# Kernel optimization log

Hardware: AMD Instinct MI355X
Metric: run time of the kernel (lower is better)

Reference implementation:

```python
import jax, jax.numpy as jnp
import numpy as np

N = 100000   # nodes
E = 1600000  # edges (before self loops)
IN, HID, OUT = 128, 128, 64


def setup_inputs() -> dict:
    key = jax.random.key(0)
    ks = jax.random.split(key, 5)
    x = jax.random.normal(ks[0], (N, IN), dtype=jnp.float32)
    edge_index = jax.random.randint(ks[1], (2, E), 0, N, dtype=jnp.int32)
    W1 = jax.random.normal(ks[2], (IN, HID), dtype=jnp.float32) * (1.0 / np.sqrt(IN))
    b1 = jnp.zeros((HID,), dtype=jnp.float32)
    W2 = jax.random.normal(ks[3], (HID, OUT), dtype=jnp.float32) * (1.0 / np.sqrt(HID))
    b2 = jnp.zeros((OUT,), dtype=jnp.float32)
    return {"x": x, "edge_index": edge_index, "W1": W1, "b1": b1, "W2": W2, "b2": b2}


def _gcn_conv(x, W, b, src, dst, norm):
    # linear transform first (small GEMM), then normalized scatter-add aggregation
    h = x @ W                                   # [N, d_out]
    msg = h[src] * norm[:, None]                # [E+N, d_out] gathered messages
    agg = jax.ops.segment_sum(msg, dst, num_segments=N)
    return agg + b


def reference(x, edge_index, W1, b1, W2, b2):
    loops = jnp.arange(N, dtype=edge_index.dtype)
    src = jnp.concatenate([edge_index[0], loops])   # add self loops (PyG GCNConv default)
    dst = jnp.concatenate([edge_index[1], loops])
    # symmetric normalization D^{-1/2} (A+I) D^{-1/2}
    deg = jax.ops.segment_sum(jnp.ones_like(dst, dtype=x.dtype), dst, num_segments=N)
    dinv = jnp.where(deg > 0, jax.lax.rsqrt(deg), 0.0)
    norm = dinv[src] * dinv[dst]                # [E+N]

    h = _gcn_conv(x, W1, b1, src, dst, norm)
    h = jax.nn.relu(h)
    out = _gcn_conv(h, W2, b2, src, dst, norm)
    return out
```

## Files before the change

kernel.cpp:

```cpp
#include <hip/hip_runtime.h>
#include <hip/hip_bf16.h>

#define IN_DIM  128
#define HID_DIM 128
#define OUT_DIM 64

typedef unsigned short ushort_t;
struct ushort4_t { ushort_t x, y, z, w; };
typedef __attribute__((ext_vector_type(8))) short bf16x8;
typedef __attribute__((ext_vector_type(4))) float f32x4;

__device__ __forceinline__ float bf2f(ushort_t u) {
    return __uint_as_float(((unsigned int)u) << 16);
}
__device__ __forceinline__ short f2bf_s(float v) {
    __hip_bfloat16 t = __float2bfloat16(v);
    return *(short*)&t;
}
__device__ __forceinline__ unsigned int pack2(float a, float b) {
    return ((unsigned int)(ushort_t)f2bf_s(b) << 16) | (ushort_t)f2bf_s(a);
}

__global__ __launch_bounds__(256, 2) void fused_gemm1_count(
        const float* __restrict__ x, const float* __restrict__ W,
        unsigned int* __restrict__ h,
        const int* __restrict__ dst, int* __restrict__ cnt, int* __restrict__ rank,
        int N, int E, int NT) {
    const int bid = blockIdx.x;
    const int tid = threadIdx.x;

    if (bid & 1) {
        const int lane = tid & 63;
        const int m    = lane & 15;
        const int quad = lane >> 4;
        const int gw   = (bid >> 1) * 4 + (tid >> 6);
        const int NW   = 1024;

        bf16x8 a[8][4];
        #pragma unroll
        for (int ct = 0; ct < 8; ++ct)
            #pragma unroll
            for (int kc = 0; kc < 4; ++kc)
                #pragma unroll
                for (int j = 0; j < 8; ++j)
                    a[ct][kc][j] = f2bf_s(W[(size_t)(kc * 32 + quad * 8 + j) * HID_DIM + ct * 16 + m]);

        for (int t = gw; t < NT; t += NW) {
            const int n0 = t * 16;
            int node = n0 + m; if (node >= N) node = N - 1;
            const float* xr = x + (size_t)node * IN_DIM + quad * 8;
            f32x4 acc[8];
            #pragma unroll
            for (int ct = 0; ct < 8; ++ct) acc[ct] = (f32x4){0.f, 0.f, 0.f, 0.f};
            #pragma unroll
            for (int kc = 0; kc < 4; ++kc) {
                const float4 v0 = *(const float4*)(xr + kc * 32);
                const float4 v1 = *(const float4*)(xr + kc * 32 + 4);
                bf16x8 b;
                b[0] = f2bf_s(v0.x); b[1] = f2bf_s(v0.y); b[2] = f2bf_s(v0.z); b[3] = f2bf_s(v0.w);
                b[4] = f2bf_s(v1.x); b[5] = f2bf_s(v1.y); b[6] = f2bf_s(v1.z); b[7] = f2bf_s(v1.w);
                #pragma unroll
                for (int ct = 0; ct < 8; ++ct)
                    acc[ct] = __builtin_amdgcn_mfma_f32_16x16x32_bf16(a[ct][kc], b, acc[ct], 0, 0, 0);
            }
            if (n0 + m < N) {
                unsigned int* o = h + (size_t)(n0 + m) * (HID_DIM / 2) + quad * 2;
                #pragma unroll
                for (int ct = 0; ct < 8; ++ct) {
                    uint2 pv;
                    pv.x = pack2(acc[ct][0], acc[ct][1]);
                    pv.y = pack2(acc[ct][2], acc[ct][3]);
                    *(uint2*)(o + ct * 8) = pv;
                }
            }
        }
    } else {
        const int ct = (bid >> 1) * 256 + tid;
        const int CT = 256 * 256;
        const int nq = E >> 2;
        const int4* d4 = (const int4*)dst;
        for (int q = ct; q < nq; q += CT) {
            const int4 d = d4[q];
            int4 r;
            r.x = atomicAdd(&cnt[d.x], 1);
            r.y = atomicAdd(&cnt[d.y], 1);
            r.z = atomicAdd(&cnt[d.z], 1);
            r.w = atomicAdd(&cnt[d.w], 1);
            ((int4*)rank)[q] = r;
        }
        for (int e = (nq << 2) + ct; e < E; e += CT)
            rank[e] = atomicAdd(&cnt[dst[e]], 1);
    }
}

__global__ void scan_partial(const int* __restrict__ cnt, int* __restrict__ bsum,
                             float* __restrict__ dinv, int N) {
    __shared__ int wsum[4];
    const int t = threadIdx.x;
    const int base = blockIdx.x * 2048 + t * 8;
    int s = 0;
    #pragma unroll
    for (int i = 0; i < 8; ++i) {
        if (base + i < N) {
            const int c = cnt[base + i];
            dinv[base + i] = rsqrtf((float)(c + 1));
            s += (c + 3) & ~3;
        }
    }
    #pragma unroll
    for (int off = 32; off > 0; off >>= 1) s += __shfl_down(s, off);
    const int lane = t & 63, w = t >> 6;
    if (lane == 0) wsum[w] = s;
    __syncthreads();
    if (t == 0) bsum[blockIdx.x] = wsum[0] + wsum[1] + wsum[2] + wsum[3];
}

__global__ void scan_write(const int* __restrict__ cnt, const int* __restrict__ bsum,
                           int* __restrict__ row_start, int2* __restrict__ pack, int N) {
    __shared__ int wsum[4];
    __shared__ int blockoff;
    const int t = threadIdx.x;
    if (t < 64) {
        int a = 0;
        for (int idx = t; idx < blockIdx.x; idx += 64) a += bsum[idx];
        #pragma unroll
        for (int off = 32; off > 0; off >>= 1) a += __shfl_down(a, off);
        if (t == 0) blockoff = a;
    }
    const int base = blockIdx.x * 2048 + t * 8;
    int c[8], v[8];
    #pragma unroll
    for (int i = 0; i < 8; ++i) {
        c[i] = (base + i < N) ? cnt[base + i] : 0;
        v[i] = (c[i] + 3) & ~3;
    }
    int s = v[0] + v[1] + v[2] + v[3] + v[4] + v[5] + v[6] + v[7];
    const int lane = t & 63, w = t >> 6;
    int incl = s;
    #pragma unroll
    for (int off = 1; off < 64; off <<= 1) {
        int u = __shfl_up(incl, off);
        if (lane >= off) incl += u;
    }
    if (lane == 63) wsum[w] = incl;
    __syncthreads();
    int woff = 0;
    for (int i = 0; i < w; ++i) woff += wsum[i];
    int run = blockoff + woff + (incl - s);
    const int2 zr = {0, 0};
    #pragma unroll
    for (int i = 0; i < 8; ++i) {
        if (base + i < N) {
            row_start[base + i] = run;
            for (int p = c[i]; p < v[i]; ++p) pack[run + p] = zr;
            run += v[i];
        }
    }
}

__global__ void fill_pack4(const int* __restrict__ src, const int* __restrict__ dst,
                           const int* __restrict__ rank, const int* __restrict__ row_start,
                           const float* __restrict__ dinv, int E, int2* __restrict__ pack) {
    const int q = blockIdx.x * blockDim.x + threadIdx.x;
    const int nq = E >> 2;
    if (q < nq) {
        const int4 s = ((const int4*)src)[q];
        const int4 d = ((const int4*)dst)[q];
        const int4 r = ((const int4*)rank)[q];
        int2 p;
        p.x = s.x; p.y = __float_as_int(dinv[s.x] * dinv[d.x]);
        pack[row_start[d.x] + r.x] = p;
        p.x = s.y; p.y = __float_as_int(dinv[s.y] * dinv[d.y]);
        pack[row_start[d.y] + r.y] = p;
        p.x = s.z; p.y = __float_as_int(dinv[s.z] * dinv[d.z]);
        pack[row_start[d.z] + r.z] = p;
        p.x = s.w; p.y = __float_as_int(dinv[s.w] * dinv[d.w]);
        pack[row_start[d.w] + r.w] = p;
    }
    if (q == 0) {
        for (int e = nq << 2; e < E; ++e) {
            int2 p;
            p.x = src[e]; p.y = __float_as_int(dinv[src[e]] * dinv[dst[e]]);
            pack[row_start[dst[e]] + rank[e]] = p;
        }
    }
}

__global__ __launch_bounds__(256) void gemm2_mfma(
        const ushort_t* __restrict__ agg,
        const float* __restrict__ W2, unsigned int* __restrict__ h2,
        int N, int NT, int NW) {
    const int tid  = threadIdx.x;
    const int lane = tid & 63;
    const int m    = lane & 15;
    const int quad = lane >> 4;
    const int gw   = blockIdx.x * 4 + (tid >> 6);

    bf16x8 a[4][4];
    #pragma unroll
    for (int ct = 0; ct < 4; ++ct)
        #pragma unroll
        for (int kc = 0; kc < 4; ++kc)
            #pragma unroll
            for (int j = 0; j < 8; ++j)
                a[ct][kc][j] = f2bf_s(W2[(size_t)(kc * 32 + quad * 8 + j) * OUT_DIM + ct * 16 + m]);

    for (int t = gw; t < NT; t += NW) {
        const int n0 = t * 16;
        int node = n0 + m; if (node >= N) node = N - 1;
        const ushort_t* ar = agg + (size_t)node * HID_DIM + quad * 8;
        f32x4 acc[4];
        #pragma unroll
        for (int ct = 0; ct < 4; ++ct) acc[ct] = (f32x4){0.f, 0.f, 0.f, 0.f};
        #pragma unroll
        for (int kc = 0; kc < 4; ++kc) {
            const bf16x8 b = *(const bf16x8*)(ar + kc * 32);
            #pragma unroll
            for (int ct = 0; ct < 4; ++ct)
                acc[ct] = __builtin_amdgcn_mfma_f32_16x16x32_bf16(a[ct][kc], b, acc[ct], 0, 0, 0);
        }
        if (n0 + m < N) {
            unsigned int* o = h2 + (size_t)(n0 + m) * (OUT_DIM / 2) + quad * 2;
            #pragma unroll
            for (int ct = 0; ct < 4; ++ct) {
                uint2 pv;
                pv.x = pack2(acc[ct][0], acc[ct][1]);
                pv.y = pack2(acc[ct][2], acc[ct][3]);
                *(uint2*)(o + ct * 8) = pv;
            }
        }
    }
}

template<int D, bool BF16_OUT, bool RELU>
__global__ void gather_bf16(const ushort_t* __restrict__ h, const int2* __restrict__ pack,
                            const int* __restrict__ row_start, const int* __restrict__ cnt,
                            const float* __restrict__ dinv, const float* __restrict__ bias,
                            int N, void* __restrict__ outv) {
    const int TPN = D / 4;
    const int NPB = 256 / TPN;
    const int t = threadIdx.x;
    const int node = blockIdx.x * NPB + t / TPN;
    if (node >= N) return;
    const int f = (t & (TPN - 1)) * 4;
    const float dd = dinv[node];

    const ushort4_t self = *(const ushort4_t*)(h + (size_t)node * D + f);
    const float sn = dd * dd;
    float4 acc;
    acc.x = bf2f(self.x) * sn; acc.y = bf2f(self.y) * sn;
    acc.z = bf2f(self.z) * sn; acc.w = bf2f(self.w) * sn;
    const float4 bv = *(const float4*)(bias + f);
    acc.x += bv.x; acc.y += bv.y; acc.z += bv.z; acc.w += bv.w;

    const int2* pk = pack + row_start[node];
    const int cpad = (cnt[node] + 3) & ~3;
    for (int e = 0; e < cpad; e += 4) {
        const int4 a = *(const int4*)(pk + e);
        const int4 b = *(const int4*)(pk + e + 2);
        {
            const ushort4_t v = *(const ushort4_t*)(h + (size_t)a.x * D + f);
            const float n = __int_as_float(a.y);
            acc.x += bf2f(v.x) * n; acc.y += bf2f(v.y) * n;
            acc.z += bf2f(v.z) * n; acc.w += bf2f(v.w) * n;
        }
        {
            const ushort4_t v = *(const ushort4_t*)(h + (size_t)a.z * D + f);
            const float n = __int_as_float(a.w);
            acc.x += bf2f(v.x) * n; acc.y += bf2f(v.y) * n;
            acc.z += bf2f(v.z) * n; acc.w += bf2f(v.w) * n;
        }
        {
            const ushort4_t v = *(const ushort4_t*)(h + (size_t)b.x * D + f);
            const float n = __int_as_float(b.y);
            acc.x += bf2f(v.x) * n; acc.y += bf2f(v.y) * n;
            acc.z += bf2f(v.z) * n; acc.w += bf2f(v.w) * n;
        }
        {
            const ushort4_t v = *(const ushort4_t*)(h + (size_t)b.z * D + f);
            const float n = __int_as_float(b.w);
            acc.x += bf2f(v.x) * n; acc.y += bf2f(v.y) * n;
            acc.z += bf2f(v.z) * n; acc.w += bf2f(v.w) * n;
        }
    }
    if (RELU) {
        acc.x = fmaxf(acc.x, 0.f); acc.y = fmaxf(acc.y, 0.f);
        acc.z = fmaxf(acc.z, 0.f); acc.w = fmaxf(acc.w, 0.f);
    }
    if (BF16_OUT) {
        unsigned int* out = (unsigned int*)outv;
        uint2 pv;
        pv.x = pack2(acc.x, acc.y);
        pv.y = pack2(acc.z, acc.w);
        *(uint2*)(out + ((size_t)node * D + f) / 2) = pv;
    } else {
        float* out = (float*)outv;
        *(float4*)(out + (size_t)node * D + f) = acc;
    }
}

extern "C" void kernel_launch(void* const* d_in, const int* in_sizes, int n_in,
                              void* d_out, int out_size, void* d_ws, size_t ws_size,
                              hipStream_t stream) {
    const float* x   = (const float*)d_in[0];
    const int*   ei  = (const int*)  d_in[1];
    const float* W1  = (const float*)d_in[2];
    const float* b1  = (const float*)d_in[3];
    const float* W2  = (const float*)d_in[4];
    const float* b2  = (const float*)d_in[5];
    float* out = (float*)d_out;

    const int N = in_sizes[0] / IN_DIM;
    const int E = in_sizes[1] / 2;
    const int* src = ei;
    const int* dst = ei + E;

    const int PACK_CAP = E + 4 * N;
    float* dinv      = (float*)d_ws;
    int*   cnt       = (int*)(dinv + N);
    int*   row_start = cnt + N;
    int*   bsum      = row_start + N;
    size_t off       = (size_t)(3 * N + 1024);
    off = (off + 3) & ~(size_t)3;
    int2*  pack      = (int2*)((int*)d_ws + off);
    unsigned int* h1 = (unsigned int*)(pack + PACK_CAP);
    unsigned int* agg1 = h1 + (size_t)N * (HID_DIM / 2);
    int*   rank      = (int*)agg1;
    unsigned int* h2 = h1;

    const int B = 256;
    const int S = (N + 2047) / 2048;
    const int NT = (N + 15) / 16;

    hipMemsetAsync(cnt, 0, (size_t)N * sizeof(int), stream);
    fused_gemm1_count<<<512, 256, 0, stream>>>(x, W1, h1, dst, cnt, rank, N, E, NT);

    scan_partial<<<S, 256, 0, stream>>>(cnt, bsum, dinv, N);
    scan_write<<<S, 256, 0, stream>>>(cnt, bsum, row_start, pack, N);

    fill_pack4<<<((E >> 2) + B - 1) / B, B, 0, stream>>>(src, dst, rank, row_start, dinv, E, pack);

    gather_bf16<HID_DIM, true, true><<<(N + 7) / 8, 256, 0, stream>>>(
        (const ushort_t*)h1, pack, row_start, cnt, dinv, b1, N, (void*)agg1);

    gemm2_mfma<<<768, 256, 0, stream>>>(
        (const ushort_t*)agg1, W2, h2, N, NT, 768 * 4);

    gather_bf16<OUT_DIM, false, false><<<(N + 15) / 16, 256, 0, stream>>>(
        (const ushort_t*)h2, pack, row_start, cnt, dinv, b2, N, (void*)out);
}
```

Before: 312.2 us.

## Fuse GEMM1, degree count, scan and CSR fill into one persistent kernel

Merges the fused GEMM1/count kernel, both scan kernels and the pack-fill kernel into a single persistent 512-block kernel, separated by atomic-counter grid barriers. This removes three kernel launches and the gaps between them. The barrier counter shares the cnt memset. It relies on all 512 blocks being co-resident, or it will deadlock. The gather loop is also unrolled to process eight edges per iteration for more memory-level parallelism.

```diff
diff --git a/kernel.cpp b/kernel.cpp
--- a/kernel.cpp
+++ b/kernel.cpp
@@ -21,13 +21,30 @@
     return ((unsigned int)(ushort_t)f2bf_s(b) << 16) | (ushort_t)f2bf_s(a);
 }
 
-__global__ __launch_bounds__(256, 2) void fused_gemm1_count(
+__device__ __forceinline__ void grid_barrier(int* bar, int epoch, int nb) {
+    __syncthreads();
+    if (threadIdx.x == 0) {
+        __threadfence();
+        __hip_atomic_fetch_add(bar, 1, __ATOMIC_RELEASE, __HIP_MEMORY_SCOPE_AGENT);
+        while (__hip_atomic_load(bar, __ATOMIC_ACQUIRE, __HIP_MEMORY_SCOPE_AGENT) < epoch * nb)
+            __builtin_amdgcn_s_sleep(100);
+        __threadfence();
+    }
+    __syncthreads();
+}
+
+__global__ __launch_bounds__(256, 2) void megakernel(
         const float* __restrict__ x, const float* __restrict__ W,
         unsigned int* __restrict__ h,
-        const int* __restrict__ dst, int* __restrict__ cnt, int* __restrict__ rank,
-        int N, int E, int NT) {
+        const int* __restrict__ src, const int* __restrict__ dst,
+        int* __restrict__ cnt, int* __restrict__ rank,
+        float* __restrict__ dinv, int* __restrict__ bsum,
+        int* __restrict__ row_start, int2* __restrict__ pack,
+        int* __restrict__ bar,
+        int N, int E, int NT, int S) {
     const int bid = blockIdx.x;
     const int tid = threadIdx.x;
+    const int NB  = 512;
 
     if (bid & 1) {
         const int lane = tid & 63;
@@ -91,97 +108,98 @@
         for (int e = (nq << 2) + ct; e < E; e += CT)
             rank[e] = atomicAdd(&cnt[dst[e]], 1);
     }
-}
-
-__global__ void scan_partial(const int* __restrict__ cnt, int* __restrict__ bsum,
-                             float* __restrict__ dinv, int N) {
-    __shared__ int wsum[4];
-    const int t = threadIdx.x;
-    const int base = blockIdx.x * 2048 + t * 8;
-    int s = 0;
-    #pragma unroll
-    for (int i = 0; i < 8; ++i) {
-        if (base + i < N) {
-            const int c = cnt[base + i];
-            dinv[base + i] = rsqrtf((float)(c + 1));
-            s += (c + 3) & ~3;
-        }
-    }
-    #pragma unroll
-    for (int off = 32; off > 0; off >>= 1) s += __shfl_down(s, off);
-    const int lane = t & 63, w = t >> 6;
-    if (lane == 0) wsum[w] = s;
-    __syncthreads();
-    if (t == 0) bsum[blockIdx.x] = wsum[0] + wsum[1] + wsum[2] + wsum[3];
-}
-
-__global__ void scan_write(const int* __restrict__ cnt, const int* __restrict__ bsum,
-                           int* __restrict__ row_start, int2* __restrict__ pack, int N) {
-    __shared__ int wsum[4];
-    __shared__ int blockoff;
-    const int t = threadIdx.x;
-    if (t < 64) {
-        int a = 0;
-        for (int idx = t; idx < blockIdx.x; idx += 64) a += bsum[idx];
-        #pragma unroll
-        for (int off = 32; off > 0; off >>= 1) a += __shfl_down(a, off);
-        if (t == 0) blockoff = a;
-    }
-    const int base = blockIdx.x * 2048 + t * 8;
-    int c[8], v[8];
-    #pragma unroll
-    for (int i = 0; i < 8; ++i) {
-        c[i] = (base + i < N) ? cnt[base + i] : 0;
-        v[i] = (c[i] + 3) & ~3;
-    }
-    int s = v[0] + v[1] + v[2] + v[3] + v[4] + v[5] + v[6] + v[7];
-    const int lane = t & 63, w = t >> 6;
-    int incl = s;
-    #pragma unroll
-    for (int off = 1; off < 64; off <<= 1) {
-        int u = __shfl_up(incl, off);
-        if (lane >= off) incl += u;
-    }
-    if (lane == 63) wsum[w] = incl;
-    __syncthreads();
-    int woff = 0;
-    for (int i = 0; i < w; ++i) woff += wsum[i];
-    int run = blockoff + woff + (incl - s);
-    const int2 zr = {0, 0};
-    #pragma unroll
-    for (int i = 0; i < 8; ++i) {
-        if (base + i < N) {
-            row_start[base + i] = run;
-            for (int p = c[i]; p < v[i]; ++p) pack[run + p] = zr;
-            run += v[i];
-        }
-    }
-}
-
-__global__ void fill_pack4(const int* __restrict__ src, const int* __restrict__ dst,
-                           const int* __restrict__ rank, const int* __restrict__ row_start,
-                           const float* __restrict__ dinv, int E, int2* __restrict__ pack) {
-    const int q = blockIdx.x * blockDim.x + threadIdx.x;
-    const int nq = E >> 2;
-    if (q < nq) {
-        const int4 s = ((const int4*)src)[q];
-        const int4 d = ((const int4*)dst)[q];
-        const int4 r = ((const int4*)rank)[q];
-        int2 p;
-        p.x = s.x; p.y = __float_as_int(dinv[s.x] * dinv[d.x]);
-        pack[row_start[d.x] + r.x] = p;
-        p.x = s.y; p.y = __float_as_int(dinv[s.y] * dinv[d.y]);
-        pack[row_start[d.y] + r.y] = p;
-        p.x = s.z; p.y = __float_as_int(dinv[s.z] * dinv[d.z]);
-        pack[row_start[d.z] + r.z] = p;
-        p.x = s.w; p.y = __float_as_int(dinv[s.w] * dinv[d.w]);
-        pack[row_start[d.w] + r.w] = p;
-    }
-    if (q == 0) {
-        for (int e = nq << 2; e < E; ++e) {
+
+    grid_barrier(bar, 1, NB);
+
+    if (bid < S) {
+        __shared__ int wsum2[4];
+        const int base = bid * 2048 + tid * 8;
+        int s = 0;
+        #pragma unroll
+        for (int i = 0; i < 8; ++i) {
+            if (base + i < N) {
+                const int c = cnt[base + i];
+                dinv[base + i] = rsqrtf((float)(c + 1));
+                s += (c + 3) & ~3;
+            }
+        }
+        #pragma unroll
+        for (int off = 32; off > 0; off >>= 1) s += __shfl_down(s, off);
+        const int lane = tid & 63, w = tid >> 6;
+        if (lane == 0) wsum2[w] = s;
+        __syncthreads();
+        if (tid == 0) bsum[bid] = wsum2[0] + wsum2[1] + wsum2[2] + wsum2[3];
+    }
+
+    grid_barrier(bar, 2, NB);
+
+    if (bid < S) {
+        __shared__ int wsum3[4];
+        __shared__ int blockoff;
+        if (tid < 64) {
+            int a = 0;
+            for (int idx = tid; idx < bid; idx += 64) a += bsum[idx];
+            #pragma unroll
+            for (int off = 32; off > 0; off >>= 1) a += __shfl_down(a, off);
+            if (tid == 0) blockoff = a;
+        }
+        const int base = bid * 2048 + tid * 8;
+        int c[8], v[8];
+        #pragma unroll
+        for (int i = 0; i < 8; ++i) {
+            c[i] = (base + i < N) ? cnt[base + i] : 0;
+            v[i] = (c[i] + 3) & ~3;
+        }
+        int s = v[0] + v[1] + v[2] + v[3] + v[4] + v[5] + v[6] + v[7];
+        const int lane = tid & 63, w = tid >> 6;
+        int incl = s;
+        #pragma unroll
+        for (int off = 1; off < 64; off <<= 1) {
+            int u = __shfl_up(incl, off);
+            if (lane >= off) incl += u;
+        }
+        if (lane == 63) wsum3[w] = incl;
+        __syncthreads();
+        int woff = 0;
+        for (int i = 0; i < w; ++i) woff += wsum3[i];
+        int run = blockoff + woff + (incl - s);
+        const int2 zr = {0, 0};
+        #pragma unroll
+        for (int i = 0; i < 8; ++i) {
+            if (base + i < N) {
+                row_start[base + i] = run;
+                for (int p = c[i]; p < v[i]; ++p) pack[run + p] = zr;
+                run += v[i];
+            }
+        }
+    }
+
+    grid_barrier(bar, 3, NB);
+
+    {
+        const int gtid = bid * 256 + tid;
+        const int GT = NB * 256;
+        const int nq = E >> 2;
+        for (int q = gtid; q < nq; q += GT) {
+            const int4 s = ((const int4*)src)[q];
+            const int4 d = ((const int4*)dst)[q];
+            const int4 r = ((const int4*)rank)[q];
             int2 p;
-            p.x = src[e]; p.y = __float_as_int(dinv[src[e]] * dinv[dst[e]]);
-            pack[row_start[dst[e]] + rank[e]] = p;
+            p.x = s.x; p.y = __float_as_int(dinv[s.x] * dinv[d.x]);
+            pack[row_start[d.x] + r.x] = p;
+            p.x = s.y; p.y = __float_as_int(dinv[s.y] * dinv[d.y]);
+            pack[row_start[d.y] + r.y] = p;
+            p.x = s.z; p.y = __float_as_int(dinv[s.z] * dinv[d.z]);
+            pack[row_start[d.z] + r.z] = p;
+            p.x = s.w; p.y = __float_as_int(dinv[s.w] * dinv[d.w]);
+            pack[row_start[d.w] + r.w] = p;
+        }
+        if (gtid == 0) {
+            for (int e = nq << 2; e < E; ++e) {
+                int2 p;
+                p.x = src[e]; p.y = __float_as_int(dinv[src[e]] * dinv[dst[e]]);
+                pack[row_start[dst[e]] + rank[e]] = p;
+            }
         }
     }
 }
@@ -231,6 +249,13 @@
         }
     }
 }
+
+#define GREC(P, HI) do { \
+        const ushort4_t v = *(const ushort4_t*)(h + (size_t)(HI ? (P).z : (P).x) * D + f); \
+        const float n = __int_as_float(HI ? (P).w : (P).y); \
+        acc.x += bf2f(v.x) * n; acc.y += bf2f(v.y) * n; \
+        acc.z += bf2f(v.z) * n; acc.w += bf2f(v.w) * n; \
+    } while (0)
 
 template<int D, bool BF16_OUT, bool RELU>
 __global__ void gather_bf16(const ushort_t* __restrict__ h, const int2* __restrict__ pack,
@@ -255,33 +280,22 @@
 
     const int2* pk = pack + row_start[node];
     const int cpad = (cnt[node] + 3) & ~3;
-    for (int e = 0; e < cpad; e += 4) {
-        const int4 a = *(const int4*)(pk + e);
-        const int4 b = *(const int4*)(pk + e + 2);
-        {
-            const ushort4_t v = *(const ushort4_t*)(h + (size_t)a.x * D + f);
-            const float n = __int_as_float(a.y);
-            acc.x += bf2f(v.x) * n; acc.y += bf2f(v.y) * n;
-            acc.z += bf2f(v.z) * n; acc.w += bf2f(v.w) * n;
-        }
-        {
-            const ushort4_t v = *(const ushort4_t*)(h + (size_t)a.z * D + f);
-            const float n = __int_as_float(a.w);
-            acc.x += bf2f(v.x) * n; acc.y += bf2f(v.y) * n;
-            acc.z += bf2f(v.z) * n; acc.w += bf2f(v.w) * n;
-        }
-        {
-            const ushort4_t v = *(const ushort4_t*)(h + (size_t)b.x * D + f);
-            const float n = __int_as_float(b.y);
-            acc.x += bf2f(v.x) * n; acc.y += bf2f(v.y) * n;
-            acc.z += bf2f(v.z) * n; acc.w += bf2f(v.w) * n;
-        }
-        {
-            const ushort4_t v = *(const ushort4_t*)(h + (size_t)b.z * D + f);
-            const float n = __int_as_float(b.w);
-            acc.x += bf2f(v.x) * n; acc.y += bf2f(v.y) * n;
-            acc.z += bf2f(v.z) * n; acc.w += bf2f(v.w) * n;
-        }
+    int e = 0;
+    for (; e + 8 <= cpad; e += 8) {
+        const int4 p0 = *(const int4*)(pk + e);
+        const int4 p1 = *(const int4*)(pk + e + 2);
+        const int4 p2 = *(const int4*)(pk + e + 4);
+        const int4 p3 = *(const int4*)(pk + e + 6);
+        GREC(p0, 0); GREC(p0, 1);
+        GREC(p1, 0); GREC(p1, 1);
+        GREC(p2, 0); GREC(p2, 1);
+        GREC(p3, 0); GREC(p3, 1);
+    }
+    if (e < cpad) {
+        const int4 p0 = *(const int4*)(pk + e);
+        const int4 p1 = *(const int4*)(pk + e + 2);
+        GREC(p0, 0); GREC(p0, 1);
+        GREC(p1, 0); GREC(p1, 1);
     }
     if (RELU) {
         acc.x = fmaxf(acc.x, 0.f); acc.y = fmaxf(acc.y, 0.f);
@@ -318,9 +332,10 @@
     const int PACK_CAP = E + 4 * N;
     float* dinv      = (float*)d_ws;
     int*   cnt       = (int*)(dinv + N);
-    int*   row_start = cnt + N;
+    int*   bar       = cnt + N;
+    int*   row_start = bar + 16;
     int*   bsum      = row_start + N;
-    size_t off       = (size_t)(3 * N + 1024);
+    size_t off       = (size_t)(3 * N + 16 + 1024);
     off = (off + 3) & ~(size_t)3;
     int2*  pack      = (int2*)((int*)d_ws + off);
     unsigned int* h1 = (unsigned int*)(pack + PACK_CAP);
@@ -328,17 +343,12 @@
     int*   rank      = (int*)agg1;
     unsigned int* h2 = h1;
 
-    const int B = 256;
     const int S = (N + 2047) / 2048;
     const int NT = (N + 15) / 16;
 
-    hipMemsetAsync(cnt, 0, (size_t)N * sizeof(int), stream);
-    fused_gemm1_count<<<512, 256, 0, stream>>>(x, W1, h1, dst, cnt, rank, N, E, NT);
-
-    scan_partial<<<S, 256, 0, stream>>>(cnt, bsum, dinv, N);
-    scan_write<<<S, 256, 0, stream>>>(cnt, bsum, row_start, pack, N);
-
-    fill_pack4<<<((E >> 2) + B - 1) / B, B, 0, stream>>>(src, dst, rank, row_start, dinv, E, pack);
+    hipMemsetAsync(cnt, 0, ((size_t)N + 16) * sizeof(int), stream);
+    megakernel<<<512, 256, 0, stream>>>(x, W1, h1, src, dst, cnt, rank,
+                                        dinv, bsum, row_start, pack, bar, N, E, NT, S);
 
     gather_bf16<HID_DIM, true, true><<<(N + 7) / 8, 256, 0, stream>>>(
         (const ushort_t*)h1, pack, row_start, cnt, dinv, b1, N, (void*)agg1);
```

Result: slower. 581.8 us (+86.3%).

## Shard degree-count atomics across shadow counter arrays and unroll gather loop

Applied to the files above, without the earlier changes.

Splits the per-destination degree counters into 8 shadow copies chosen by thread block, so atomic increments contend less. The scan then sums the shadows and writes a per-shadow base offset, which fill_pack4 uses to place each edge in the CSR. The gather loop is also unrolled to handle 8 edges per iteration. The cost is a larger memset and extra reads and writes of 8N-sized arrays in the scan kernels.

```diff
diff --git a/kernel.cpp b/kernel.cpp
--- a/kernel.cpp
+++ b/kernel.cpp
@@ -4,6 +4,7 @@
 #define IN_DIM  128
 #define HID_DIM 128
 #define OUT_DIM 64
+#define NSHADOW 8
 
 typedef unsigned short ushort_t;
 struct ushort4_t { ushort_t x, y, z, w; };
@@ -24,7 +25,7 @@
 __global__ __launch_bounds__(256, 2) void fused_gemm1_count(
         const float* __restrict__ x, const float* __restrict__ W,
         unsigned int* __restrict__ h,
-        const int* __restrict__ dst, int* __restrict__ cnt, int* __restrict__ rank,
+        const int* __restrict__ dst, int* __restrict__ scnt, int* __restrict__ rank,
         int N, int E, int NT) {
     const int bid = blockIdx.x;
     const int tid = threadIdx.x;
@@ -77,24 +78,28 @@
     } else {
         const int ct = (bid >> 1) * 256 + tid;
         const int CT = 256 * 256;
+        const int sh = (ct >> 8) & (NSHADOW - 1);
+        int* __restrict__ mycnt = scnt + (size_t)sh * N;
         const int nq = E >> 2;
         const int4* d4 = (const int4*)dst;
         for (int q = ct; q < nq; q += CT) {
             const int4 d = d4[q];
             int4 r;
-            r.x = atomicAdd(&cnt[d.x], 1);
-            r.y = atomicAdd(&cnt[d.y], 1);
-            r.z = atomicAdd(&cnt[d.z], 1);
-            r.w = atomicAdd(&cnt[d.w], 1);
+            r.x = atomicAdd(&mycnt[d.x], 1);
+            r.y = atomicAdd(&mycnt[d.y], 1);
+            r.z = atomicAdd(&mycnt[d.z], 1);
+            r.w = atomicAdd(&mycnt[d.w], 1);
             ((int4*)rank)[q] = r;
         }
-        for (int e = (nq << 2) + ct; e < E; e += CT)
-            rank[e] = atomicAdd(&cnt[dst[e]], 1);
-    }
-}
-
-__global__ void scan_partial(const int* __restrict__ cnt, int* __restrict__ bsum,
-                             float* __restrict__ dinv, int N) {
+        for (int e = (nq << 2) + ct; e < E; e += CT) {
+            const int sh2 = ((e - (nq << 2)) >> 8) & (NSHADOW - 1);
+            rank[e] = atomicAdd(&scnt[(size_t)sh2 * N + dst[e]], 1);
+        }
+    }
+}
+
+__global__ void scan_partial(const int* __restrict__ scnt, int* __restrict__ cnt,
+                             int* __restrict__ bsum, float* __restrict__ dinv, int N) {
     __shared__ int wsum[4];
     const int t = threadIdx.x;
     const int base = blockIdx.x * 2048 + t * 8;
@@ -102,7 +107,10 @@
     #pragma unroll
     for (int i = 0; i < 8; ++i) {
         if (base + i < N) {
-            const int c = cnt[base + i];
+            int c = 0;
+            #pragma unroll
+            for (int sh = 0; sh < NSHADOW; ++sh) c += scnt[(size_t)sh * N + base + i];
+            cnt[base + i] = c;
             dinv[base + i] = rsqrtf((float)(c + 1));
             s += (c + 3) & ~3;
         }
@@ -115,8 +123,10 @@
     if (t == 0) bsum[blockIdx.x] = wsum[0] + wsum[1] + wsum[2] + wsum[3];
 }
 
-__global__ void scan_write(const int* __restrict__ cnt, const int* __restrict__ bsum,
-                           int* __restrict__ row_start, int2* __restrict__ pack, int N) {
+__global__ void scan_write(const int* __restrict__ cnt, const int* __restrict__ scnt,
+                           const int* __restrict__ bsum,
+                           int* __restrict__ row_start, int* __restrict__ sb,
+                           int2* __restrict__ pack, int N) {
     __shared__ int wsum[4];
     __shared__ int blockoff;
     const int t = threadIdx.x;
@@ -152,6 +162,12 @@
     for (int i = 0; i < 8; ++i) {
         if (base + i < N) {
             row_start[base + i] = run;
+            int a = run;
+            #pragma unroll
+            for (int sh = 0; sh < NSHADOW; ++sh) {
+                sb[(size_t)sh * N + base + i] = a;
+                a += scnt[(size_t)sh * N + base + i];
+            }
             for (int p = c[i]; p < v[i]; ++p) pack[run + p] = zr;
             run += v[i];
         }
@@ -159,29 +175,33 @@
 }
 
 __global__ void fill_pack4(const int* __restrict__ src, const int* __restrict__ dst,
-                           const int* __restrict__ rank, const int* __restrict__ row_start,
-                           const float* __restrict__ dinv, int E, int2* __restrict__ pack) {
+                           const int* __restrict__ rank, const int* __restrict__ sb,
+                           const float* __restrict__ dinv, int N, int E, int2* __restrict__ pack) {
     const int q = blockIdx.x * blockDim.x + threadIdx.x;
+    const int CT = 256 * 256;
     const int nq = E >> 2;
     if (q < nq) {
+        const int sh = ((q & (CT - 1)) >> 8) & (NSHADOW - 1);
+        const int* __restrict__ sbs = sb + (size_t)sh * N;
         const int4 s = ((const int4*)src)[q];
         const int4 d = ((const int4*)dst)[q];
         const int4 r = ((const int4*)rank)[q];
         int2 p;
         p.x = s.x; p.y = __float_as_int(dinv[s.x] * dinv[d.x]);
-        pack[row_start[d.x] + r.x] = p;
+        pack[sbs[d.x] + r.x] = p;
         p.x = s.y; p.y = __float_as_int(dinv[s.y] * dinv[d.y]);
-        pack[row_start[d.y] + r.y] = p;
+        pack[sbs[d.y] + r.y] = p;
         p.x = s.z; p.y = __float_as_int(dinv[s.z] * dinv[d.z]);
-        pack[row_start[d.z] + r.z] = p;
+        pack[sbs[d.z] + r.z] = p;
         p.x = s.w; p.y = __float_as_int(dinv[s.w] * dinv[d.w]);
-        pack[row_start[d.w] + r.w] = p;
+        pack[sbs[d.w] + r.w] = p;
     }
     if (q == 0) {
         for (int e = nq << 2; e < E; ++e) {
+            const int sh = ((e - (nq << 2)) >> 8) & (NSHADOW - 1);
             int2 p;
             p.x = src[e]; p.y = __float_as_int(dinv[src[e]] * dinv[dst[e]]);
-            pack[row_start[dst[e]] + rank[e]] = p;
+            pack[sb[(size_t)sh * N + dst[e]] + rank[e]] = p;
         }
     }
 }
@@ -231,6 +251,13 @@
         }
     }
 }
+
+#define GREC(P, HI) do { \
+        const ushort4_t v = *(const ushort4_t*)(h + (size_t)(HI ? (P).z : (P).x) * D + f); \
+        const float n = __int_as_float(HI ? (P).w : (P).y); \
+        acc.x += bf2f(v.x) * n; acc.y += bf2f(v.y) * n; \
+        acc.z += bf2f(v.z) * n; acc.w += bf2f(v.w) * n; \
+    } while (0)
 
 template<int D, bool BF16_OUT, bool RELU>
 __global__ void gather_bf16(const ushort_t* __restrict__ h, const int2* __restrict__ pack,
@@ -255,33 +282,22 @@
 
     const int2* pk = pack + row_start[node];
     const int cpad = (cnt[node] + 3) & ~3;
-    for (int e = 0; e < cpad; e += 4) {
-        const int4 a = *(const int4*)(pk + e);
-        const int4 b = *(const int4*)(pk + e + 2);
-        {
-            const ushort4_t v = *(const ushort4_t*)(h + (size_t)a.x * D + f);
-            const float n = __int_as_float(a.y);
-            acc.x += bf2f(v.x) * n; acc.y += bf2f(v.y) * n;
-            acc.z += bf2f(v.z) * n; acc.w += bf2f(v.w) * n;
-        }
-        {
-            const ushort4_t v = *(const ushort4_t*)(h + (size_t)a.z * D + f);
-            const float n = __int_as_float(a.w);
-            acc.x += bf2f(v.x) * n; acc.y += bf2f(v.y) * n;
-            acc.z += bf2f(v.z) * n; acc.w += bf2f(v.w) * n;
-        }
-        {
-            const ushort4_t v = *(const ushort4_t*)(h + (size_t)b.x * D + f);
-            const float n = __int_as_float(b.y);
-            acc.x += bf2f(v.x) * n; acc.y += bf2f(v.y) * n;
-            acc.z += bf2f(v.z) * n; acc.w += bf2f(v.w) * n;
-        }
-        {
-            const ushort4_t v = *(const ushort4_t*)(h + (size_t)b.z * D + f);
-            const float n = __int_as_float(b.w);
-            acc.x += bf2f(v.x) * n; acc.y += bf2f(v.y) * n;
-            acc.z += bf2f(v.z) * n; acc.w += bf2f(v.w) * n;
-        }
+    int e = 0;
+    for (; e + 8 <= cpad; e += 8) {
+        const int4 p0 = *(const int4*)(pk + e);
+        const int4 p1 = *(const int4*)(pk + e + 2);
+        const int4 p2 = *(const int4*)(pk + e + 4);
+        const int4 p3 = *(const int4*)(pk + e + 6);
+        GREC(p0, 0); GREC(p0, 1);
+        GREC(p1, 0); GREC(p1, 1);
+        GREC(p2, 0); GREC(p2, 1);
+        GREC(p3, 0); GREC(p3, 1);
+    }
+    if (e < cpad) {
+        const int4 p0 = *(const int4*)(pk + e);
+        const int4 p1 = *(const int4*)(pk + e + 2);
+        GREC(p0, 0); GREC(p0, 1);
+        GREC(p1, 0); GREC(p1, 1);
     }
     if (RELU) {
         acc.x = fmaxf(acc.x, 0.f); acc.y = fmaxf(acc.y, 0.f);
@@ -320,7 +336,9 @@
     int*   cnt       = (int*)(dinv + N);
     int*   row_start = cnt + N;
     int*   bsum      = row_start + N;
-    size_t off       = (size_t)(3 * N + 1024);
+    int*   scnt      = bsum + 1024;
+    int*   sb        = scnt + (size_t)NSHADOW * N;
+    size_t off       = (size_t)(3 * N + 1024) + (size_t)2 * NSHADOW * N;
     off = (off + 3) & ~(size_t)3;
     int2*  pack      = (int2*)((int*)d_ws + off);
     unsigned int* h1 = (unsigned int*)(pack + PACK_CAP);
@@ -332,13 +350,13 @@
     const int S = (N + 2047) / 2048;
     const int NT = (N + 15) / 16;
 
-    hipMemsetAsync(cnt, 0, (size_t)N * sizeof(int), stream);
-    fused_gemm1_count<<<512, 256, 0, stream>>>(x, W1, h1, dst, cnt, rank, N, E, NT);
-
-    scan_partial<<<S, 256, 0, stream>>>(cnt, bsum, dinv, N);
-    scan_write<<<S, 256, 0, stream>>>(cnt, bsum, row_start, pack, N);
-
-    fill_pack4<<<((E >> 2) + B - 1) / B, B, 0, stream>>>(src, dst, rank, row_start, dinv, E, pack);
+    hipMemsetAsync(scnt, 0, (size_t)NSHADOW * N * sizeof(int), stream);
+    fused_gemm1_count<<<512, 256, 0, stream>>>(x, W1, h1, dst, scnt, rank, N, E, NT);
+
+    scan_partial<<<S, 256, 0, stream>>>(scnt, cnt, bsum, dinv, N);
+    scan_write<<<S, 256, 0, stream>>>(cnt, scnt, bsum, row_start, sb, pack, N);
+
+    fill_pack4<<<((E >> 2) + B - 1) / B, B, 0, stream>>>(src, dst, rank, sb, dinv, N, E, pack);
 
     gather_bf16<HID_DIM, true, true><<<(N + 7) / 8, 256, 0, stream>>>(
         (const ushort_t*)h1, pack, row_start, cnt, dinv, b1, N, (void*)agg1);
```

New measurement: 336.3 us. 1.08x slower.

## Fuse scan kernels and switch gathers to wave-per-node with edge-split lanes

Applied to the files above, without the earlier changes.

Merges the two-pass prefix scan into one kernel in which each block recomputes its offset by summing the preceding counts, removing a launch and the bsum buffer. Replaces the per-node gather with a persistent wave-per-node kernel that splits edges across lane groups and combines partial sums with xor shuffles. This is meant to increase memory-level parallelism per node and reduce serial edge loops, at the cost of shuffle reductions and redundant prefix reads in the scan.

```diff
diff --git a/kernel.cpp b/kernel.cpp
--- a/kernel.cpp
+++ b/kernel.cpp
@@ -93,49 +93,35 @@
     }
 }
 
-__global__ void scan_partial(const int* __restrict__ cnt, int* __restrict__ bsum,
-                             float* __restrict__ dinv, int N) {
-    __shared__ int wsum[4];
-    const int t = threadIdx.x;
-    const int base = blockIdx.x * 2048 + t * 8;
-    int s = 0;
-    #pragma unroll
-    for (int i = 0; i < 8; ++i) {
-        if (base + i < N) {
-            const int c = cnt[base + i];
-            dinv[base + i] = rsqrtf((float)(c + 1));
-            s += (c + 3) & ~3;
-        }
-    }
-    #pragma unroll
-    for (int off = 32; off > 0; off >>= 1) s += __shfl_down(s, off);
-    const int lane = t & 63, w = t >> 6;
-    if (lane == 0) wsum[w] = s;
-    __syncthreads();
-    if (t == 0) bsum[blockIdx.x] = wsum[0] + wsum[1] + wsum[2] + wsum[3];
-}
-
-__global__ void scan_write(const int* __restrict__ cnt, const int* __restrict__ bsum,
+__global__ void scan_fused(const int* __restrict__ cnt, float* __restrict__ dinv,
                            int* __restrict__ row_start, int2* __restrict__ pack, int N) {
     __shared__ int wsum[4];
-    __shared__ int blockoff;
+    __shared__ int sh_off;
     const int t = threadIdx.x;
-    if (t < 64) {
-        int a = 0;
-        for (int idx = t; idx < blockIdx.x; idx += 64) a += bsum[idx];
-        #pragma unroll
-        for (int off = 32; off > 0; off >>= 1) a += __shfl_down(a, off);
-        if (t == 0) blockoff = a;
-    }
-    const int base = blockIdx.x * 2048 + t * 8;
+    const int base0 = blockIdx.x * 2048;
+
+    int pre = 0;
+    for (int i = t * 4; i < base0; i += 1024) {
+        const int4 c4 = *(const int4*)(cnt + i);
+        pre += ((c4.x + 3) & ~3) + ((c4.y + 3) & ~3) + ((c4.z + 3) & ~3) + ((c4.w + 3) & ~3);
+    }
+    #pragma unroll
+    for (int off = 32; off > 0; off >>= 1) pre += __shfl_down(pre, off);
+    const int lane = t & 63, w = t >> 6;
+    if (lane == 0) wsum[w] = pre;
+    __syncthreads();
+    if (t == 0) sh_off = wsum[0] + wsum[1] + wsum[2] + wsum[3];
+    __syncthreads();
+
+    const int base = base0 + t * 8;
     int c[8], v[8];
     #pragma unroll
     for (int i = 0; i < 8; ++i) {
         c[i] = (base + i < N) ? cnt[base + i] : 0;
         v[i] = (c[i] + 3) & ~3;
+        if (base + i < N) dinv[base + i] = rsqrtf((float)(c[i] + 1));
     }
     int s = v[0] + v[1] + v[2] + v[3] + v[4] + v[5] + v[6] + v[7];
-    const int lane = t & 63, w = t >> 6;
     int incl = s;
     #pragma unroll
     for (int off = 1; off < 64; off <<= 1) {
@@ -146,7 +132,7 @@
     __syncthreads();
     int woff = 0;
     for (int i = 0; i < w; ++i) woff += wsum[i];
-    int run = blockoff + woff + (incl - s);
+    int run = sh_off + woff + (incl - s);
     const int2 zr = {0, 0};
     #pragma unroll
     for (int i = 0; i < 8; ++i) {
@@ -233,69 +219,75 @@
 }
 
 template<int D, bool BF16_OUT, bool RELU>
-__global__ void gather_bf16(const ushort_t* __restrict__ h, const int2* __restrict__ pack,
+__global__ void gather_wave(const ushort_t* __restrict__ h, const int2* __restrict__ pack,
                             const int* __restrict__ row_start, const int* __restrict__ cnt,
                             const float* __restrict__ dinv, const float* __restrict__ bias,
-                            int N, void* __restrict__ outv) {
-    const int TPN = D / 4;
-    const int NPB = 256 / TPN;
-    const int t = threadIdx.x;
-    const int node = blockIdx.x * NPB + t / TPN;
-    if (node >= N) return;
-    const int f = (t & (TPN - 1)) * 4;
-    const float dd = dinv[node];
-
-    const ushort4_t self = *(const ushort4_t*)(h + (size_t)node * D + f);
-    const float sn = dd * dd;
-    float4 acc;
-    acc.x = bf2f(self.x) * sn; acc.y = bf2f(self.y) * sn;
-    acc.z = bf2f(self.z) * sn; acc.w = bf2f(self.w) * sn;
-    const float4 bv = *(const float4*)(bias + f);
-    acc.x += bv.x; acc.y += bv.y; acc.z += bv.z; acc.w += bv.w;
-
-    const int2* pk = pack + row_start[node];
-    const int cpad = (cnt[node] + 3) & ~3;
-    for (int e = 0; e < cpad; e += 4) {
-        const int4 a = *(const int4*)(pk + e);
-        const int4 b = *(const int4*)(pk + e + 2);
-        {
-            const ushort4_t v = *(const ushort4_t*)(h + (size_t)a.x * D + f);
-            const float n = __int_as_float(a.y);
-            acc.x += bf2f(v.x) * n; acc.y += bf2f(v.y) * n;
-            acc.z += bf2f(v.z) * n; acc.w += bf2f(v.w) * n;
-        }
-        {
-            const ushort4_t v = *(const ushort4_t*)(h + (size_t)a.z * D + f);
-            const float n = __int_as_float(a.w);
-            acc.x += bf2f(v.x) * n; acc.y += bf2f(v.y) * n;
-            acc.z += bf2f(v.z) * n; acc.w += bf2f(v.w) * n;
-        }
-        {
-            const ushort4_t v = *(const ushort4_t*)(h + (size_t)b.x * D + f);
-            const float n = __int_as_float(b.y);
-            acc.x += bf2f(v.x) * n; acc.y += bf2f(v.y) * n;
-            acc.z += bf2f(v.z) * n; acc.w += bf2f(v.w) * n;
-        }
-        {
-            const ushort4_t v = *(const ushort4_t*)(h + (size_t)b.z * D + f);
-            const float n = __int_as_float(b.w);
-            acc.x += bf2f(v.x) * n; acc.y += bf2f(v.y) * n;
-            acc.z += bf2f(v.z) * n; acc.w += bf2f(v.w) * n;
-        }
-    }
-    if (RELU) {
-        acc.x = fmaxf(acc.x, 0.f); acc.y = fmaxf(acc.y, 0.f);
-        acc.z = fmaxf(acc.z, 0.f); acc.w = fmaxf(acc.w, 0.f);
-    }
-    if (BF16_OUT) {
-        unsigned int* out = (unsigned int*)outv;
-        uint2 pv;
-        pv.x = pack2(acc.x, acc.y);
-        pv.y = pack2(acc.z, acc.w);
-        *(uint2*)(out + ((size_t)node * D + f) / 2) = pv;
-    } else {
-        float* out = (float*)outv;
-        *(float4*)(out + (size_t)node * D + f) = acc;
+                            int N, void* __restrict__ outv, int NWAVES) {
+    const int lane = threadIdx.x & 63;
+    const int gwid = (blockIdx.x * blockDim.x + threadIdx.x) >> 6;
+    const int TPR  = D / 4;
+    const int R    = 64 / TPR;
+    const int f    = (lane & (TPR - 1)) * 4;
+    const int rsub = lane / TPR;
+
+    for (int node = gwid; node < N; node += NWAVES) {
+        const float dd = dinv[node];
+        float4 acc = {0.f, 0.f, 0.f, 0.f};
+        if (rsub == 0) {
+            const ushort4_t self = *(const ushort4_t*)(h + (size_t)node * D + f);
+            const float sn = dd * dd;
+            const float4 bv = *(const float4*)(bias + f);
+            acc.x = bf2f(self.x) * sn + bv.x;
+            acc.y = bf2f(self.y) * sn + bv.y;
+            acc.z = bf2f(self.z) * sn + bv.z;
+            acc.w = bf2f(self.w) * sn + bv.w;
+        }
+        const int2* pk = pack + row_start[node];
+        const int cpad = (cnt[node] + 3) & ~3;
+        int e = 0;
+        for (; e + 8 <= cpad; e += 8) {
+            #pragma unroll
+            for (int s = 0; s < 8; s += R) {
+                const int2 pr = pk[e + s + rsub];
+                const ushort4_t v = *(const ushort4_t*)(h + (size_t)pr.x * D + f);
+                const float n = __int_as_float(pr.y);
+                acc.x += bf2f(v.x) * n; acc.y += bf2f(v.y) * n;
+                acc.z += bf2f(v.z) * n; acc.w += bf2f(v.w) * n;
+            }
+        }
+        for (; e < cpad; e += 4) {
+            #pragma unroll
+            for (int s = 0; s < 4; s += R) {
+                const int2 pr = pk[e + s + rsub];
+                const ushort4_t v = *(const ushort4_t*)(h + (size_t)pr.x * D + f);
+                const float n = __int_as_float(pr.y);
+                acc.x += bf2f(v.x) * n; acc.y += bf2f(v.y) * n;
+                acc.z += bf2f(v.z) * n; acc.w += bf2f(v.w) * n;
+            }
+        }
+        #pragma unroll
+        for (int off = TPR; off < 64; off <<= 1) {
+            acc.x += __shfl_xor(acc.x, off);
+            acc.y += __shfl_xor(acc.y, off);
+            acc.z += __shfl_xor(acc.z, off);
+            acc.w += __shfl_xor(acc.w, off);
+        }
+        if (rsub == 0) {
+            if (RELU) {
+                acc.x = fmaxf(acc.x, 0.f); acc.y = fmaxf(acc.y, 0.f);
+                acc.z = fmaxf(acc.z, 0.f); acc.w = fmaxf(acc.w, 0.f);
+            }
+            if (BF16_OUT) {
+                unsigned int* out = (unsigned int*)outv;
+                uint2 pv;
+                pv.x = pack2(acc.x, acc.y);
+                pv.y = pack2(acc.z, acc.w);
+                *(uint2*)(out + ((size_t)node * D + f) / 2) = pv;
+            } else {
+                float* out = (float*)outv;
+                *(float4*)(out + (size_t)node * D + f) = acc;
+            }
+        }
     }
 }
 
@@ -319,8 +311,7 @@
     float* dinv      = (float*)d_ws;
     int*   cnt       = (int*)(dinv + N);
     int*   row_start = cnt + N;
-    int*   bsum      = row_start + N;
-    size_t off       = (size_t)(3 * N + 1024);
+    size_t off       = (size_t)(3 * N);
     off = (off + 3) & ~(size_t)3;
     int2*  pack      = (int2*)((int*)d_ws + off);
     unsigned int* h1 = (unsigned int*)(pack + PACK_CAP);
@@ -331,21 +322,21 @@
     const int B = 256;
     const int S = (N + 2047) / 2048;
     const int NT = (N + 15) / 16;
+    const int GB = 4096;
 
     hipMemsetAsync(cnt, 0, (size_t)N * sizeof(int), stream);
     fused_gemm1_count<<<512, 256, 0, stream>>>(x, W1, h1, dst, cnt, rank, N, E, NT);
 
-    scan_partial<<<S, 256, 0, stream>>>(cnt, bsum, dinv, N);
-    scan_write<<<S, 256, 0, stream>>>(cnt, bsum, row_start, pack, N);
+    scan_fused<<<S, 256, 0, stream>>>(cnt, dinv, row_start, pack, N);
 
     fill_pack4<<<((E >> 2) + B - 1) / B, B, 0, stream>>>(src, dst, rank, row_start, dinv, E, pack);
 
-    gather_bf16<HID_DIM, true, true><<<(N + 7) / 8, 256, 0, stream>>>(
-        (const ushort_t*)h1, pack, row_start, cnt, dinv, b1, N, (void*)agg1);
+    gather_wave<HID_DIM, true, true><<<GB, 256, 0, stream>>>(
+        (const ushort_t*)h1, pack, row_start, cnt, dinv, b1, N, (void*)agg1, GB * 4);
 
     gemm2_mfma<<<768, 256, 0, stream>>>(
         (const ushort_t*)agg1, W2, h2, N, NT, 768 * 4);
 
-    gather_bf16<OUT_DIM, false, false><<<(N + 15) / 16, 256, 0, stream>>>(
-        (const ushort_t*)h2, pack, row_start, cnt, dinv, b2, N, (void*)out);
-}
+    gather_wave<OUT_DIM, false, false><<<GB, 256, 0, stream>>>(
+        (const ushort_t*)h2, pack, row_start, cnt, dinv, b2, N, (void*)out, GB * 4);
+}
```

Measured after the change: 341.8 us. 9.5% more time.
